# Kernel tuning notes

Measured on AMD Instinct MI355X. Metric: run time of the kernel, lower is better.

The kernel has to match this reference:

```python
import jax, jax.numpy as jnp
import numpy as np

N, E, IN, H0, H1 = 50000, 1600000, 64, 64, 128


def _gcn(h, W, b, row, col):
    # PyG GCNConv, add_self_loops=False, unit edge weights:
    # out[col] += d^{-1/2}[row] * d^{-1/2}[col] * (h @ W)[row]; bias added after aggregation
    n = h.shape[0]
    deg = jnp.zeros((n,), h.dtype).at[col].add(jnp.ones((row.shape[0],), h.dtype))
    dinv = jnp.where(deg > 0, jax.lax.rsqrt(jnp.maximum(deg, 1e-12)), 0.0)
    norm = (dinv[row] * dinv[col])[:, None]  # [E,1]
    m = h @ W  # transform before propagate (small GEMM)
    out = jnp.zeros((n, W.shape[1]), h.dtype).at[col].add(norm * m[row])
    return out + b


def _bn(h, g, b):
    # BatchNorm1d training-mode math (biased variance), eps=1e-5
    mu = h.mean(0)
    var = ((h - mu) ** 2).mean(0)
    return g * (h - mu) * jax.lax.rsqrt(var + 1e-5) + b


def _san(h):
    return jnp.nan_to_num(h, nan=0.0, posinf=100.0, neginf=-100.0)


def _slice(x, ei, W0, b0, W1, b1, res1, g0, be0, g1, be1):
    row, col = ei[0], ei[1]
    # layer 0: conv -> bn -> relu -> (dropout=eval identity) -> residual (Identity, 64==64) -> nan_to_num
    h1 = _san(jax.nn.relu(_bn(_gcn(x, W0, b0, row, col), g0, be0)) + x)
    # layer 1 (last): conv -> bn -> residual (Linear proj 64->128, no bias) -> nan_to_num
    h2 = _san(_bn(_gcn(h1, W1, b1, row, col), g1, be1) + h1 @ res1)
    return h2


def setup_inputs() -> dict:
    k = jax.random.split(jax.random.key(0), 16)
    f = lambda kk, sh, s: jax.random.normal(kk, sh, jnp.float32) * s
    return {
        "x": f(k[0], (N, IN), 1.0),
        "edge_index0": jax.random.randint(k[1], (2, E), 0, N),
        "edge_index1": jax.random.randint(k[2], (2, E), 0, N),
        "w0_s0": f(k[3], (IN, H0), 0.1), "b0_s0": jnp.zeros((H0,), jnp.float32),
        "w1_s0": f(k[4], (H0, H1), 0.1), "b1_s0": jnp.zeros((H1,), jnp.float32),
        "res1_s0": f(k[5], (H0, H1), 0.1),
        "w0_s1": f(k[6], (IN, H0), 0.1), "b0_s1": jnp.zeros((H0,), jnp.float32),
        "w1_s1": f(k[7], (H0, H1), 0.1), "b1_s1": jnp.zeros((H1,), jnp.float32),
        "res1_s1": f(k[8], (H0, H1), 0.1),
        "bn_g0": jnp.ones((H0,), jnp.float32), "bn_b0": jnp.zeros((H0,), jnp.float32),
        "bn_g1": jnp.ones((H1,), jnp.float32), "bn_b1": jnp.zeros((H1,), jnp.float32),
        "fc1_w": f(k[9], (2 * H1, H1), 0.1), "fc1_b": jnp.zeros((H1,), jnp.float32),
        "fc2_w": f(k[10], (H1, 2), 0.1), "fc2_b": jnp.zeros((2,), jnp.float32),
    }


def reference(x, edge_index0, edge_index1,
              w0_s0, b0_s0, w1_s0, b1_s0, res1_s0,
              w0_s1, b0_s1, w1_s1, b1_s1, res1_s1,
              bn_g0, bn_b0, bn_g1, bn_b1,
              fc1_w, fc1_b, fc2_w, fc2_b):
    out0 = _slice(x, edge_index0, w0_s0, b0_s0, w1_s0, b1_s0, res1_s0, bn_g0, bn_b0, bn_g1, bn_b1)
    out1 = _slice(x, edge_index1, w0_s1, b0_s1, w1_s1, b1_s1, res1_s1, bn_g0, bn_b0, bn_g1, bn_b1)
    combined = jnp.concatenate([out0, out1], axis=1)  # [N, 2*H1]
    h = jax.nn.relu(combined @ fc1_w + fc1_b)  # dropout is eval-mode identity
    logits = h @ fc2_w + fc2_b
    return logits, jax.nn.softmax(logits, axis=1)
```

## Files before the change

### kernel.cpp

```cpp
#include <hip/hip_runtime.h>
#include <hip/hip_bf16.h>
#include <math.h>


typedef short v8s __attribute__((ext_vector_type(8)));
typedef float f32x4 __attribute__((ext_vector_type(4)));

#define BSTRIDE 10240

__device__ __forceinline__ float sanf(float v) {
    if (v != v) return 0.f;
    if (isinf(v)) return v > 0.f ? 100.f : -100.f;
    return v;
}

__device__ __forceinline__ unsigned short bf16of(float v) {
    __hip_bfloat16 h = __float2bfloat16(v);
    return *(unsigned short*)&h;
}
__device__ __forceinline__ unsigned pack2(float lo, float hi) {
    return (unsigned)bf16of(lo) | ((unsigned)bf16of(hi) << 16);
}
__device__ __forceinline__ float uflo(unsigned u) { return __uint_as_float(u << 16); }
__device__ __forceinline__ float ufhi(unsigned u) { return __uint_as_float(u & 0xFFFF0000u); }
__device__ __forceinline__ float fofbf16(unsigned short u) {
    return __uint_as_float(((unsigned)u) << 16);
}

__device__ __forceinline__ void packone(const float* __restrict__ src, unsigned* __restrict__ dst,
                                        int L, int Khalf, int F) {
    int c = L / Khalf, kp = L - c * Khalf;
    dst[L] = pack2(src[(2 * kp) * F + c], src[(2 * kp + 1) * F + c]);
}

__global__ __launch_bounds__(256) void prep_kernel(const float* __restrict__ w0_0,
                                                   const float* __restrict__ w0_1,
                                                   const float* __restrict__ w1_0,
                                                   const float* __restrict__ w1_1,
                                                   const float* __restrict__ r_0,
                                                   const float* __restrict__ r_1,
                                                   const float* __restrict__ fc1,
                                                   unsigned* __restrict__ wpk,
                                                   int* __restrict__ bcnt,
                                                   float* __restrict__ sums) {
    int gid = blockIdx.x * 256 + threadIdx.x;
    if (gid < 512) bcnt[gid] = 0;
    if (gid < 8192) sums[gid] = 0.f;
    if (gid < 2048)       packone(w0_0, wpk + 0,     gid - 0,     32, 64);
    else if (gid < 4096)  packone(w0_1, wpk + 2048,  gid - 2048,  32, 64);
    else if (gid < 8192)  packone(w1_0, wpk + 4096,  gid - 4096,  32, 128);
    else if (gid < 12288) packone(w1_1, wpk + 8192,  gid - 8192,  32, 128);
    else if (gid < 16384) packone(r_0,  wpk + 12288, gid - 12288, 32, 128);
    else if (gid < 20480) packone(r_1,  wpk + 16384, gid - 16384, 32, 128);
    else if (gid < 36864) packone(fc1,  wpk + 20480, gid - 20480, 128, 128);
}


__global__ __launch_bounds__(512) void kC_bin(const int* __restrict__ ei0,
                                              const int* __restrict__ ei1,
                                              int* __restrict__ bcnt,
                                              unsigned* __restrict__ binned,
                                              int E, int n) {
    __shared__ int cnt[512];
    __shared__ int base[512];
    int t = threadIdx.x;
    cnt[t] = 0;
    int E2 = 2 * E;
    int e0 = blockIdx.x * 8192;
    unsigned pk[16];
    int bk[16];
    __syncthreads();
#pragma unroll
    for (int j = 0; j < 16; ++j) {
        int ge = e0 + t + j * 512;
        bk[j] = -1;
        if (ge < E2) {
            int slice = ge >= E;
            const int* ei = slice ? ei1 : ei0;
            int e = ge - slice * E;
            int col = ei[E + e], row = ei[e];
            int gcol = slice * n + col;
            bk[j] = gcol >> 8;
            pk[j] = (unsigned)row | (((unsigned)gcol & 255u) << 16);
            atomicAdd(&cnt[bk[j]], 1);
        }
    }
    __syncthreads();
    {
        int c = cnt[t];
        base[t] = c ? atomicAdd(&bcnt[t], c) : 0;
    }
    __syncthreads();
    cnt[t] = 0;
    __syncthreads();
#pragma unroll
    for (int j = 0; j < 16; ++j) {
        if (bk[j] >= 0) {
            int loc = atomicAdd(&cnt[bk[j]], 1);
            int off = base[bk[j]] + loc;
            if (off < BSTRIDE) binned[(size_t)bk[j] * BSTRIDE + off] = pk[j];
        }
    }
}

__global__ __launch_bounds__(256) void kB_scan(const int* __restrict__ bcnt,
                                               int* __restrict__ bstart, int NB) {
    __shared__ int tmp[256];
    int t = threadIdx.x, carry = 0;
    for (int bse = 0; bse < NB; bse += 256) {
        int i = bse + t;
        int v = (i < NB) ? bcnt[i] : 0;
        tmp[t] = v;
        __syncthreads();
        for (int off = 1; off < 256; off <<= 1) {
            int u = (t >= off) ? tmp[t - off] : 0;
            __syncthreads();
            tmp[t] += u;
            __syncthreads();
        }
        if (i < NB) bstart[i] = tmp[t] - v + carry;
        carry += tmp[255];
        __syncthreads();
    }
    if (t == 0) bstart[NB] = carry;
}

__global__ __launch_bounds__(512) void kD_build(const unsigned* __restrict__ binned,
                                                const int* __restrict__ bstart,
                                                int* __restrict__ rowptr,
                                                float* __restrict__ dinv,
                                                unsigned short* __restrict__ csr,
                                                int n2, int NB) {
    __shared__ int cnt[256];
    __shared__ int scn[256];
    __shared__ int cur[256];
    int b = blockIdx.x, t = threadIdx.x;
    int s = bstart[b], e = bstart[b + 1];
    int m = e - s;
    const unsigned* seg = binned + (size_t)b * BSTRIDE;
    if (t < 256) cnt[t] = 0;
    __syncthreads();
    for (int i = t; i < m; i += 512) atomicAdd(&cnt[(seg[i] >> 16) & 255], 1);
    __syncthreads();
    int v = (t < 256) ? cnt[t] : 0;
    if (t < 256) scn[t] = v;
    __syncthreads();
    for (int off = 1; off < 256; off <<= 1) {
        int u = (t < 256 && t >= off) ? scn[t - off] : 0;
        __syncthreads();
        if (t < 256) scn[t] += u;
        __syncthreads();
    }
    if (t < 256) {
        int excl = scn[t] - v;
        int gcol = b * 256 + t;
        if (gcol < n2) {
            rowptr[gcol] = s + excl;
            dinv[gcol] = v > 0 ? rsqrtf((float)v) : 0.f;
        }
        cur[t] = excl;
    }
    __syncthreads();
    for (int i = t; i < m; i += 512) {
        unsigned p = seg[i];
        int cl = (p >> 16) & 255;
        int pos = s + atomicAdd(&cur[cl], 1);
        csr[pos] = (unsigned short)(p & 0xFFFFu);
    }
    if (b == 0 && t == 0) rowptr[n2] = bstart[NB];
}


__global__ __launch_bounds__(256) void prescale_bf(const float* __restrict__ x,
                                                   const float* __restrict__ dinv,
                                                   unsigned short* __restrict__ xsb,
                                                   int n64, int n) {
    int i8 = (blockIdx.x * 256 + threadIdx.x) * 8;
    if (i8 >= n64) return;
    int row = i8 >> 6;
    float4 v0 = *(const float4*)&x[i8];
    float4 v1 = *(const float4*)&x[i8 + 4];
    float d0 = dinv[row], d1 = dinv[n + row];
    uint4 o0, o1;
    o0.x = pack2(v0.x * d0, v0.y * d0); o0.y = pack2(v0.z * d0, v0.w * d0);
    o0.z = pack2(v1.x * d0, v1.y * d0); o0.w = pack2(v1.z * d0, v1.w * d0);
    o1.x = pack2(v0.x * d1, v0.y * d1); o1.y = pack2(v0.z * d1, v0.w * d1);
    o1.z = pack2(v1.x * d1, v1.y * d1); o1.w = pack2(v1.z * d1, v1.w * d1);
    *(uint4*)&xsb[i8] = o0;
    *(uint4*)&xsb[n64 + i8] = o1;
}

#define LOAD8(U, IDX)                                                       \
    do {                                                                    \
        _Pragma("unroll") for (int j = 0; j < 8; ++j) {                     \
            int r = __shfl((IDX), j, 8);                                    \
            (U)[j] = *(const uint4*)&mb[(size_t)r * 64 + l * 8];            \
        }                                                                   \
    } while (0)
#define ZPAD8(U, BB)                                                        \
    do {                                                                    \
        _Pragma("unroll") for (int j = 0; j < 8; ++j)                       \
            if ((BB) + j >= e) { (U)[j].x = 0; (U)[j].y = 0;                \
                                 (U)[j].z = 0; (U)[j].w = 0; }              \
    } while (0)
#define ACC8(U)                                                             \
    do {                                                                    \
        _Pragma("unroll") for (int j = 0; j < 8; ++j) {                     \
            a0 += uflo((U)[j].x); a1 += ufhi((U)[j].x);                     \
            a2 += uflo((U)[j].y); a3 += ufhi((U)[j].y);                     \
            a4 += uflo((U)[j].z); a5 += ufhi((U)[j].z);                     \
            a6 += uflo((U)[j].w); a7 += ufhi((U)[j].w);                     \
        }                                                                   \
    } while (0)

__global__ __launch_bounds__(256) void gatherbf_kernel(const int* __restrict__ rowptr,
                                                       const unsigned short* __restrict__ csr,
                                                       const unsigned short* __restrict__ xsb,
                                                       const float* __restrict__ dinv,
                                                       unsigned short* __restrict__ outb,
                                                       int n) {
    int blk = blockIdx.x;
    int xcd = blk & 7;
    int slice = (xcd >= 4) ? 1 : 0;
    int rank = (blk >> 3) * 4 + (xcd & 3);
    int nodeLocal = rank * 32 + (threadIdx.x >> 3);
    if (nodeLocal >= n) return;
    int node = slice * n + nodeLocal;
    int l = threadIdx.x & 7;
    const unsigned short* mb = xsb + (size_t)slice * n * 64;
    int s = rowptr[node], e = rowptr[node + 1];
    float a0 = 0.f, a1 = 0.f, a2 = 0.f, a3 = 0.f, a4 = 0.f, a5 = 0.f, a6 = 0.f, a7 = 0.f;
    uint4 uA[8], uB[8];
    int b = s;
    if (b + 8 <= e) {
        int ia = csr[b + l];
        LOAD8(uA, ia);
        int bB = b + 8;
        int ib = (bB + l < e) ? (int)csr[bB + l] : 0;
        while (true) {
            bool hasB = (bB < e);
            if (hasB) {
                LOAD8(uB, ib);
                if (bB + 8 > e) ZPAD8(uB, bB);
            }
            int bA2 = bB + 8;
            if (bA2 < e) ia = (bA2 + l < e) ? (int)csr[bA2 + l] : 0;
            ACC8(uA);
            if (!hasB) break;
            bool hasA2 = (bA2 < e);
            if (hasA2) {
                LOAD8(uA, ia);
                if (bA2 + 8 > e) ZPAD8(uA, bA2);
            }
            int bB2 = bA2 + 8;
            if (bB2 < e) ib = (bB2 + l < e) ? (int)csr[bB2 + l] : 0;
            ACC8(uB);
            if (!hasA2) break;
            bB = bB2;
        }
    } else if (b < e) {
        int ia = (b + l < e) ? (int)csr[b + l] : 0;
        LOAD8(uA, ia);
        ZPAD8(uA, b);
        ACC8(uA);
    }
    float d = dinv[node];
    uint4 o;
    o.x = pack2(a0 * d, a1 * d);
    o.y = pack2(a2 * d, a3 * d);
    o.z = pack2(a4 * d, a5 * d);
    o.w = pack2(a6 * d, a7 * d);
    *(uint4*)&outb[(size_t)node * 64 + l * 8] = o;
}


template <int F>
__global__ __launch_bounds__(256) void mfma_gemmb(const unsigned short* __restrict__ Ab,
                                                  const unsigned* __restrict__ WT0,
                                                  const unsigned* __restrict__ WT1,
                                                  unsigned short* __restrict__ Cb,
                                                  float* __restrict__ sums_base,
                                                  int roff, int n) {
    constexpr int NC = F / 16;
    __shared__ float ls[2 * F];
    __shared__ unsigned short stb[64 * F];
    int BPS = (n + 63) >> 6;
    int slice = blockIdx.x >= BPS;
    int sb = blockIdx.x - slice * BPS;
    const unsigned* WT = slice ? WT1 : WT0;
    int row0 = slice * n + sb * 64;
    int rows = min(64, n - sb * 64);
    for (int i = threadIdx.x; i < 2 * F; i += 256) ls[i] = 0.f;
    int w = threadIdx.x >> 6, lane = threadIdx.x & 63, q = lane >> 4, ln = lane & 15;
    const unsigned* A32 = (const unsigned*)Ab;
    size_t arow = (size_t)(row0 + 16 * w + ln) * 32;
    v8s af0 = *(const v8s*)&A32[arow + q * 4];
    v8s af1 = *(const v8s*)&A32[arow + 16 + q * 4];
    f32x4 acc[NC];
#pragma unroll
    for (int ct = 0; ct < NC; ++ct) acc[ct] = {0.f, 0.f, 0.f, 0.f};
#pragma unroll
    for (int ct = 0; ct < NC; ++ct) {
        v8s b0 = *(const v8s*)&WT[(ct * 16 + ln) * 32 + q * 4];
        v8s b1 = *(const v8s*)&WT[(ct * 16 + ln) * 32 + 16 + q * 4];
        acc[ct] = __builtin_amdgcn_mfma_f32_16x16x32_bf16(af0, b0, acc[ct], 0, 0, 0);
        acc[ct] = __builtin_amdgcn_mfma_f32_16x16x32_bf16(af1, b1, acc[ct], 0, 0, 0);
    }
    __syncthreads();
#pragma unroll
    for (int ct = 0; ct < NC; ++ct) {
        float s1 = 0.f, s2 = 0.f;
        int cc = ct * 16 + ln;
#pragma unroll
        for (int i = 0; i < 4; ++i) {
            int r = 16 * w + q * 4 + i;
            stb[r * F + (cc ^ ((r & 7) << 3))] = bf16of(acc[ct][i]);
            if (r < rows) {
                float v = acc[ct][i];
                s1 += v;
                s2 += v * v;
            }
        }
        s1 += __shfl_xor(s1, 16); s1 += __shfl_xor(s1, 32);
        s2 += __shfl_xor(s2, 16); s2 += __shfl_xor(s2, 32);
        if (q == 0) {
            atomicAdd(&ls[cc], s1);
            atomicAdd(&ls[F + cc], s2);
        }
    }
    __syncthreads();
    {
        constexpr int CPT = F / 4;
        int rr = threadIdx.x >> 2, sg = threadIdx.x & 3;
        if (rr < rows) {
            int swz = (rr & 7) << 3;
            int cb = sg * CPT;
            uint4* dst = (uint4*)(Cb + (size_t)(row0 + rr) * F + cb);
#pragma unroll
            for (int jj = 0; jj < CPT / 8; ++jj)
                dst[jj] = *(const uint4*)&stb[rr * F + ((cb + jj * 8) ^ swz)];
        }
    }
    if (threadIdx.x < F) {
        float* dst = sums_base + (blockIdx.x & 7) * 1024 + roff + slice * 2 * F;
        unsafeAtomicAdd(&dst[threadIdx.x], ls[threadIdx.x]);
        unsafeAtomicAdd(&dst[F + threadIdx.x], ls[F + threadIdx.x]);
    }
}

__global__ __launch_bounds__(256) void mfma_apply1(const unsigned short* __restrict__ h1b,
                                                   const unsigned short* __restrict__ Tb,
                                                   const unsigned* __restrict__ RT0,
                                                   const unsigned* __restrict__ RT1,
                                                   const float* __restrict__ scsh,
                                                   unsigned short* __restrict__ comb, int n) {
    __shared__ float st[64 * 128];
    int BPS = (n + 63) >> 6;
    int slice = blockIdx.x >= BPS;
    int sb = blockIdx.x - slice * BPS;
    const unsigned* WT = slice ? RT1 : RT0;
    int row0 = slice * n + sb * 64;
    int rows = min(64, n - sb * 64);
    int w = threadIdx.x >> 6, lane = threadIdx.x & 63, q = lane >> 4, ln = lane & 15;
    const unsigned* A32 = (const unsigned*)h1b;
    size_t arow = (size_t)(row0 + 16 * w + ln) * 32;
    v8s af0 = *(const v8s*)&A32[arow + q * 4];
    v8s af1 = *(const v8s*)&A32[arow + 16 + q * 4];
    f32x4 acc[8];
#pragma unroll
    for (int ct = 0; ct < 8; ++ct) acc[ct] = {0.f, 0.f, 0.f, 0.f};
#pragma unroll
    for (int ct = 0; ct < 8; ++ct) {
        v8s b0 = *(const v8s*)&WT[(ct * 16 + ln) * 32 + q * 4];
        v8s b1 = *(const v8s*)&WT[(ct * 16 + ln) * 32 + 16 + q * 4];
        acc[ct] = __builtin_amdgcn_mfma_f32_16x16x32_bf16(af0, b0, acc[ct], 0, 0, 0);
        acc[ct] = __builtin_amdgcn_mfma_f32_16x16x32_bf16(af1, b1, acc[ct], 0, 0, 0);
    }
#pragma unroll
    for (int ct = 0; ct < 8; ++ct) {
        int cc = ct * 16 + ln;
#pragma unroll
        for (int i = 0; i < 4; ++i) {
            int r = 16 * w + q * 4 + i;
            st[r * 128 + (cc ^ ((r & 7) << 2))] = acc[ct][i];
        }
    }
    __syncthreads();
    int rr = threadIdx.x >> 2, sg = threadIdx.x & 3;
    if (rr >= rows) return;
    int swz = (rr & 7) << 2;
    int rg = row0 + rr;
    const uint4* tbp = (const uint4*)(Tb + (size_t)rg * 128 + sg * 32);
    const float* scb = scsh + slice * 256 + sg * 32;
    uint4* outp = (uint4*)(comb + (size_t)(rg - slice * n) * 256 + slice * 128 + sg * 32);
#pragma unroll
    for (int jj = 0; jj < 4; ++jj) {
        uint4 t = tbp[jj];
        int base = sg * 32 + jj * 8;
        float4 a0 = *(const float4*)&st[rr * 128 + (base ^ swz)];
        float4 a1 = *(const float4*)&st[rr * 128 + ((base + 4) ^ swz)];
        float4 s0 = *(const float4*)&scb[jj * 8];
        float4 s1 = *(const float4*)&scb[jj * 8 + 4];
        float4 h0 = *(const float4*)&scb[128 + jj * 8];
        float4 h1v = *(const float4*)&scb[128 + jj * 8 + 4];
        float o0 = sanf(fmaf(uflo(t.x), s0.x, h0.x) + a0.x);
        float o1 = sanf(fmaf(ufhi(t.x), s0.y, h0.y) + a0.y);
        float o2 = sanf(fmaf(uflo(t.y), s0.z, h0.z) + a0.z);
        float o3 = sanf(fmaf(ufhi(t.y), s0.w, h0.w) + a0.w);
        float o4 = sanf(fmaf(uflo(t.z), s1.x, h1v.x) + a1.x);
        float o5 = sanf(fmaf(ufhi(t.z), s1.y, h1v.y) + a1.y);
        float o6 = sanf(fmaf(uflo(t.w), s1.z, h1v.z) + a1.z);
        float o7 = sanf(fmaf(ufhi(t.w), s1.w, h1v.w) + a1.w);
        uint4 ov;
        ov.x = pack2(o0, o1);
        ov.y = pack2(o2, o3);
        ov.z = pack2(o4, o5);
        ov.w = pack2(o6, o7);
        outp[jj] = ov;
    }
}

__global__ __launch_bounds__(256) void mfma_head_fc2(const unsigned short* __restrict__ comb,
                                                     const unsigned* __restrict__ FT,
                                                     const float* __restrict__ bias,
                                                     const float* __restrict__ w2,
                                                     const float* __restrict__ b2,
                                                     float* __restrict__ out, int n) {
    int row0 = blockIdx.x * 64;
    int rows = min(64, n - row0);
    int w = threadIdx.x >> 6, lane = threadIdx.x & 63, q = lane >> 4, ln = lane & 15;
    const unsigned* A32 = (const unsigned*)comb;
    size_t arow = (size_t)(row0 + 16 * w + ln) * 128;
    f32x4 acc[8];
#pragma unroll
    for (int ct = 0; ct < 8; ++ct) acc[ct] = {0.f, 0.f, 0.f, 0.f};
#pragma unroll
    for (int kt = 0; kt < 4; ++kt) {
        v8s af0 = *(const v8s*)&A32[arow + kt * 32 + q * 4];
        v8s af1 = *(const v8s*)&A32[arow + kt * 32 + 16 + q * 4];
#pragma unroll
        for (int ct = 0; ct < 8; ++ct) {
            v8s b0 = *(const v8s*)&FT[(ct * 16 + ln) * 128 + kt * 32 + q * 4];
            v8s b1 = *(const v8s*)&FT[(ct * 16 + ln) * 128 + kt * 32 + 16 + q * 4];
            acc[ct] = __builtin_amdgcn_mfma_f32_16x16x32_bf16(af0, b0, acc[ct], 0, 0, 0);
            acc[ct] = __builtin_amdgcn_mfma_f32_16x16x32_bf16(af1, b1, acc[ct], 0, 0, 0);
        }
    }
    float p0[4] = {0.f, 0.f, 0.f, 0.f}, p1[4] = {0.f, 0.f, 0.f, 0.f};
#pragma unroll
    for (int ct = 0; ct < 8; ++ct) {
        int c = ct * 16 + ln;
        float bi = bias[c];
        float w20 = w2[c * 2], w21 = w2[c * 2 + 1];
#pragma unroll
        for (int i = 0; i < 4; ++i) {
            float h = fmaxf(acc[ct][i] + bi, 0.f);
            p0[i] = fmaf(h, w20, p0[i]);
            p1[i] = fmaf(h, w21, p1[i]);
        }
    }
#pragma unroll
    for (int i = 0; i < 4; ++i) {
#pragma unroll
        for (int msk = 1; msk < 16; msk <<= 1) {
            p0[i] += __shfl_xor(p0[i], msk);
            p1[i] += __shfl_xor(p1[i], msk);
        }
    }
    if (ln == 0) {
        float bb0 = b2[0], bb1 = b2[1];
#pragma unroll
        for (int i = 0; i < 4; ++i) {
            int r = 16 * w + q * 4 + i;
            if (r >= rows) continue;
            int R = row0 + r;
            float l0 = p0[i] + bb0, l1 = p1[i] + bb1;
            float mx = fmaxf(l0, l1);
            float e0 = expf(l0 - mx), e1 = expf(l1 - mx);
            float inv = 1.0f / (e0 + e1);
            out[(size_t)R * 2] = l0;
            out[(size_t)R * 2 + 1] = l1;
            out[(size_t)2 * n + R * 2] = e0 * inv;
            out[(size_t)2 * n + R * 2 + 1] = e1 * inv;
        }
    }
}


template <int F>
__global__ void bnfinal_kernel(const float* __restrict__ sums_base, int roff,
                               const float* __restrict__ g,
                               const float* __restrict__ be, float* __restrict__ scsh, int n) {
    int f = threadIdx.x;
    if (f >= F) return;
    int slice = blockIdx.x;
    float s1 = 0.f, s2 = 0.f;
#pragma unroll
    for (int r = 0; r < 8; ++r) {
        const float* src = sums_base + r * 1024 + roff + slice * 2 * F;
        s1 += src[f];
        s2 += src[F + f];
    }
    float inv_n = 1.0f / (float)n;
    float mu = s1 * inv_n;
    float var = fmaxf(s2 * inv_n - mu * mu, 0.f);
    float scale = g[f] * rsqrtf(var + 1e-5f);
    scsh[slice * 2 * F + f] = scale;
    scsh[slice * 2 * F + F + f] = be[f] - mu * scale;
}

__global__ __launch_bounds__(256) void apply0_kernel(const unsigned short* __restrict__ t0b,
                                                     const float* __restrict__ x,
                                                     const float* __restrict__ scsh,
                                                     const float* __restrict__ dinv,
                                                     unsigned short* __restrict__ h1b,
                                                     unsigned short* __restrict__ h1sb,
                                                     int n64, int total) {
    int i8 = (blockIdx.x * 256 + threadIdx.x) * 8;
    if (i8 >= total) return;
    int slice = i8 >= n64;
    int f0 = i8 & 63;
    const float* sc = scsh + slice * 128;
    uint4 t = *(const uint4*)&t0b[i8];
    const float* xp = x + (i8 - slice * n64);
    float4 x0 = *(const float4*)xp;
    float4 x1 = *(const float4*)(xp + 4);
    float4 s0 = *(const float4*)&sc[f0];
    float4 s1 = *(const float4*)&sc[f0 + 4];
    float4 g0 = *(const float4*)&sc[64 + f0];
    float4 g1 = *(const float4*)&sc[64 + f0 + 4];
    float d = dinv[i8 >> 6];
    float tv[8] = {uflo(t.x), ufhi(t.x), uflo(t.y), ufhi(t.y),
                   uflo(t.z), ufhi(t.z), uflo(t.w), ufhi(t.w)};
    float sa[8] = {s0.x, s0.y, s0.z, s0.w, s1.x, s1.y, s1.z, s1.w};
    float sh[8] = {g0.x, g0.y, g0.z, g0.w, g1.x, g1.y, g1.z, g1.w};
    float xv[8] = {x0.x, x0.y, x0.z, x0.w, x1.x, x1.y, x1.z, x1.w};
    unsigned po[4], ps[4];
#pragma unroll
    for (int j = 0; j < 4; ++j) {
        float a = sanf(fmaxf(fmaf(tv[2 * j], sa[2 * j], sh[2 * j]), 0.f) + xv[2 * j]);
        float b = sanf(fmaxf(fmaf(tv[2 * j + 1], sa[2 * j + 1], sh[2 * j + 1]), 0.f) + xv[2 * j + 1]);
        po[j] = pack2(a, b);
        ps[j] = pack2(a * d, b * d);
    }
    *(uint4*)&h1b[i8] = *(uint4*)po;
    *(uint4*)&h1sb[i8] = *(uint4*)ps;
}

static inline int cdiv(int a, int b) { return (a + b - 1) / b; }

extern "C" void kernel_launch(void* const* d_in, const int* in_sizes, int n_in,
                              void* d_out, int out_size, void* d_ws, size_t ws_size,
                              hipStream_t stream) {
    const float* x       = (const float*)d_in[0];
    const int*   ei0     = (const int*)d_in[1];
    const int*   ei1     = (const int*)d_in[2];
    const float* w0_s0   = (const float*)d_in[3];
    const float* w1_s0   = (const float*)d_in[5];
    const float* res1_s0 = (const float*)d_in[7];
    const float* w0_s1   = (const float*)d_in[8];
    const float* w1_s1   = (const float*)d_in[10];
    const float* res1_s1 = (const float*)d_in[12];
    const float* bn_g0   = (const float*)d_in[13];
    const float* bn_b0   = (const float*)d_in[14];
    const float* bn_g1   = (const float*)d_in[15];
    const float* bn_b1   = (const float*)d_in[16];
    const float* fc1_w   = (const float*)d_in[17];
    const float* fc1_b   = (const float*)d_in[18];
    const float* fc2_w   = (const float*)d_in[19];
    const float* fc2_b   = (const float*)d_in[20];
    float* out = (float*)d_out;

    int n = in_sizes[0] / 64;
    int E = in_sizes[1] / 2;
    int n2 = 2 * n, E2 = 2 * E;
    int n64 = n * 64;
    int NB = cdiv(n2, 256);
    int BPS = cdiv(n, 64);
    int GB = 8 * cdiv(cdiv(n, 32), 4);

    float* X1 = (float*)d_ws;
    float* S  = X1 + (size_t)n2 * 64;
    unsigned short* Gb   = (unsigned short*)(S + (size_t)n2 * 64);
    unsigned short* h1b  = Gb + (size_t)n2 * 64;
    unsigned short* comb = h1b + (size_t)n2 * 64;
    unsigned short* xsb  = comb + (size_t)n * 256;
    float* dinv = (float*)(xsb + (size_t)n * 128);
    float* sums = dinv + n2;
    float* scsh = sums + 8192;
    unsigned* wpk = (unsigned*)(scsh + 512);
    unsigned short* csr = (unsigned short*)(wpk + 36864);
    int* rowptr = (int*)(csr + (size_t)E2);
    int* bcnt   = rowptr + (n2 + 1);
    int* bstart = bcnt + 512;
    unsigned short* t0b = (unsigned short*)X1;
    unsigned short* Tb  = (unsigned short*)X1;
    unsigned* binned = (unsigned*)comb;
    unsigned short* h1sb = (unsigned short*)S;
    unsigned* w0T0 = wpk + 0,    *w0T1 = wpk + 2048;
    unsigned* w1T0 = wpk + 4096, *w1T1 = wpk + 8192;
    unsigned* rT0  = wpk + 12288,*rT1  = wpk + 16384;
    unsigned* fT   = wpk + 20480;

    prep_kernel<<<144, 256, 0, stream>>>(w0_s0, w0_s1, w1_s0, w1_s1,
                                         res1_s0, res1_s1, fc1_w, wpk, bcnt, sums);
    kC_bin<<<cdiv(E2, 8192), 512, 0, stream>>>(ei0, ei1, bcnt, binned, E, n);
    kB_scan<<<1, 256, 0, stream>>>(bcnt, bstart, NB);
    kD_build<<<NB, 512, 0, stream>>>(binned, bstart, rowptr, dinv, csr, n2, NB);

    prescale_bf<<<cdiv(n64, 2048), 256, 0, stream>>>(x, dinv, xsb, n64, n);
    gatherbf_kernel<<<GB, 256, 0, stream>>>(rowptr, csr, xsb, dinv, Gb, n);
    mfma_gemmb<64><<<2 * BPS, 256, 0, stream>>>(Gb, w0T0, w0T1, t0b, sums, 512, n);
    bnfinal_kernel<64><<<2, 64, 0, stream>>>(sums, 512, bn_g0, bn_b0, scsh, n);
    apply0_kernel<<<cdiv(2 * n64, 2048), 256, 0, stream>>>(t0b, x, scsh, dinv, h1b, h1sb, n64, 2 * n64);

    gatherbf_kernel<<<GB, 256, 0, stream>>>(rowptr, csr, h1sb, dinv, Gb, n);
    mfma_gemmb<128><<<2 * BPS, 256, 0, stream>>>(Gb, w1T0, w1T1, Tb, sums, 0, n);
    bnfinal_kernel<128><<<2, 128, 0, stream>>>(sums, 0, bn_g1, bn_b1, scsh, n);
    mfma_apply1<<<2 * BPS, 256, 0, stream>>>(h1b, Tb, rT0, rT1, scsh, comb, n);

    mfma_head_fc2<<<BPS, 256, 0, stream>>>(comb, fT, fc1_b, fc2_w, fc2_b, out, n);
}
```

Before: 363.8 us.

## Fuse gather into GEMM, fold scan into CSR build and BN finalize into consumers

The edge gather now writes its aggregated tile into LDS and feeds the MFMA GEMM directly, so the bf16 intermediate no longer round-trips through global memory. The single-block bucket scan kernel is removed: every kD_build block recomputes a 512-entry prefix over the bucket counts. The BatchNorm finalize kernels are also removed; apply0 and apply1 compute scale and shift from the partial sums themselves. Together these cut five launches and one global buffer pass, at the cost of redundant per-block prefix and stat work and more LDS per GEMM block, which may lower occupancy.

```diff
diff --git a/kernel.cpp b/kernel.cpp
--- a/kernel.cpp
+++ b/kernel.cpp
@@ -103,39 +103,27 @@
     }
 }
 
-__global__ __launch_bounds__(256) void kB_scan(const int* __restrict__ bcnt,
-                                               int* __restrict__ bstart, int NB) {
-    __shared__ int tmp[256];
-    int t = threadIdx.x, carry = 0;
-    for (int bse = 0; bse < NB; bse += 256) {
-        int i = bse + t;
-        int v = (i < NB) ? bcnt[i] : 0;
-        tmp[t] = v;
-        __syncthreads();
-        for (int off = 1; off < 256; off <<= 1) {
-            int u = (t >= off) ? tmp[t - off] : 0;
-            __syncthreads();
-            tmp[t] += u;
-            __syncthreads();
-        }
-        if (i < NB) bstart[i] = tmp[t] - v + carry;
-        carry += tmp[255];
-        __syncthreads();
-    }
-    if (t == 0) bstart[NB] = carry;
-}
-
 __global__ __launch_bounds__(512) void kD_build(const unsigned* __restrict__ binned,
-                                                const int* __restrict__ bstart,
+                                                const int* __restrict__ bcnt,
                                                 int* __restrict__ rowptr,
                                                 float* __restrict__ dinv,
                                                 unsigned short* __restrict__ csr,
                                                 int n2, int NB) {
+    __shared__ int pref[512];
     __shared__ int cnt[256];
     __shared__ int scn[256];
     __shared__ int cur[256];
     int b = blockIdx.x, t = threadIdx.x;
-    int s = bstart[b], e = bstart[b + 1];
+    pref[t] = (t < NB) ? bcnt[t] : 0;
+    __syncthreads();
+    for (int off = 1; off < 512; off <<= 1) {
+        int u = (t >= off) ? pref[t - off] : 0;
+        __syncthreads();
+        pref[t] += u;
+        __syncthreads();
+    }
+    int s = (b > 0) ? pref[b - 1] : 0;
+    int e = pref[b];
     int m = e - s;
     const unsigned* seg = binned + (size_t)b * BSTRIDE;
     if (t < 256) cnt[t] = 0;
@@ -167,7 +155,7 @@
         int pos = s + atomicAdd(&cur[cl], 1);
         csr[pos] = (unsigned short)(p & 0xFFFFu);
     }
-    if (b == 0 && t == 0) rowptr[n2] = bstart[NB];
+    if (b == 0 && t == 0) rowptr[n2] = pref[NB - 1];
 }
 
 
@@ -213,21 +201,12 @@
         }                                                                   \
     } while (0)
 
-__global__ __launch_bounds__(256) void gatherbf_kernel(const int* __restrict__ rowptr,
-                                                       const unsigned short* __restrict__ csr,
-                                                       const unsigned short* __restrict__ xsb,
-                                                       const float* __restrict__ dinv,
-                                                       unsigned short* __restrict__ outb,
-                                                       int n) {
-    int blk = blockIdx.x;
-    int xcd = blk & 7;
-    int slice = (xcd >= 4) ? 1 : 0;
-    int rank = (blk >> 3) * 4 + (xcd & 3);
-    int nodeLocal = rank * 32 + (threadIdx.x >> 3);
-    if (nodeLocal >= n) return;
-    int node = slice * n + nodeLocal;
-    int l = threadIdx.x & 7;
-    const unsigned short* mb = xsb + (size_t)slice * n * 64;
+__device__ __forceinline__ void gather_node(const int* __restrict__ rowptr,
+                                            const unsigned short* __restrict__ csr,
+                                            const unsigned short* __restrict__ mb,
+                                            const float* __restrict__ dinv,
+                                            int node, int l,
+                                            unsigned short* __restrict__ dstrow) {
     int s = rowptr[node], e = rowptr[node + 1];
     float a0 = 0.f, a1 = 0.f, a2 = 0.f, a3 = 0.f, a4 = 0.f, a5 = 0.f, a6 = 0.f, a7 = 0.f;
     uint4 uA[8], uB[8];
@@ -270,32 +249,49 @@
     o.y = pack2(a2 * d, a3 * d);
     o.z = pack2(a4 * d, a5 * d);
     o.w = pack2(a6 * d, a7 * d);
-    *(uint4*)&outb[(size_t)node * 64 + l * 8] = o;
-}
-
+    *(uint4*)&dstrow[l * 8] = o;
+}
 
 template <int F>
-__global__ __launch_bounds__(256) void mfma_gemmb(const unsigned short* __restrict__ Ab,
-                                                  const unsigned* __restrict__ WT0,
-                                                  const unsigned* __restrict__ WT1,
-                                                  unsigned short* __restrict__ Cb,
-                                                  float* __restrict__ sums_base,
-                                                  int roff, int n) {
+__global__ __launch_bounds__(256) void gather_gemmb(const int* __restrict__ rowptr,
+                                                    const unsigned short* __restrict__ csr,
+                                                    const unsigned short* __restrict__ xsb,
+                                                    const float* __restrict__ dinv,
+                                                    const unsigned* __restrict__ WT0,
+                                                    const unsigned* __restrict__ WT1,
+                                                    unsigned short* __restrict__ Cb,
+                                                    float* __restrict__ sums_base,
+                                                    int roff, int n, int BPS) {
     constexpr int NC = F / 16;
+    __shared__ unsigned short at[64 * 72];
+    __shared__ unsigned short stb[64 * F];
     __shared__ float ls[2 * F];
-    __shared__ unsigned short stb[64 * F];
-    int BPS = (n + 63) >> 6;
-    int slice = blockIdx.x >= BPS;
-    int sb = blockIdx.x - slice * BPS;
+    int blk = blockIdx.x;
+    int xcd = blk & 7;
+    int slice = (xcd >= 4) ? 1 : 0;
+    int sb = (blk >> 3) * 4 + (xcd & 3);
+    if (sb >= BPS) return;
     const unsigned* WT = slice ? WT1 : WT0;
     int row0 = slice * n + sb * 64;
     int rows = min(64, n - sb * 64);
+    int grp = threadIdx.x >> 3, l = threadIdx.x & 7;
+    const unsigned short* mb = xsb + (size_t)slice * n * 64;
+#pragma unroll
+    for (int half = 0; half < 2; ++half) {
+        int lr = grp + half * 32;
+        if (lr < rows) {
+            gather_node(rowptr, csr, mb, dinv, row0 + lr, l, &at[lr * 72]);
+        } else {
+            uint4 z; z.x = 0; z.y = 0; z.z = 0; z.w = 0;
+            *(uint4*)&at[lr * 72 + l * 8] = z;
+        }
+    }
     for (int i = threadIdx.x; i < 2 * F; i += 256) ls[i] = 0.f;
+    __syncthreads();
     int w = threadIdx.x >> 6, lane = threadIdx.x & 63, q = lane >> 4, ln = lane & 15;
-    const unsigned* A32 = (const unsigned*)Ab;
-    size_t arow = (size_t)(row0 + 16 * w + ln) * 32;
-    v8s af0 = *(const v8s*)&A32[arow + q * 4];
-    v8s af1 = *(const v8s*)&A32[arow + 16 + q * 4];
+    int arow = (16 * w + ln) * 72;
+    v8s af0 = *(const v8s*)&at[arow + q * 8];
+    v8s af1 = *(const v8s*)&at[arow + 32 + q * 8];
     f32x4 acc[NC];
 #pragma unroll
     for (int ct = 0; ct < NC; ++ct) acc[ct] = {0.f, 0.f, 0.f, 0.f};
@@ -306,7 +302,6 @@
         acc[ct] = __builtin_amdgcn_mfma_f32_16x16x32_bf16(af0, b0, acc[ct], 0, 0, 0);
         acc[ct] = __builtin_amdgcn_mfma_f32_16x16x32_bf16(af1, b1, acc[ct], 0, 0, 0);
     }
-    __syncthreads();
 #pragma unroll
     for (int ct = 0; ct < NC; ++ct) {
         float s1 = 0.f, s2 = 0.f;
@@ -352,16 +347,35 @@
                                                    const unsigned short* __restrict__ Tb,
                                                    const unsigned* __restrict__ RT0,
                                                    const unsigned* __restrict__ RT1,
-                                                   const float* __restrict__ scsh,
+                                                   const float* __restrict__ sums_base,
+                                                   const float* __restrict__ g,
+                                                   const float* __restrict__ be,
                                                    unsigned short* __restrict__ comb, int n) {
     __shared__ float st[64 * 128];
+    __shared__ float scl[256];
     int BPS = (n + 63) >> 6;
     int slice = blockIdx.x >= BPS;
     int sb = blockIdx.x - slice * BPS;
     const unsigned* WT = slice ? RT1 : RT0;
     int row0 = slice * n + sb * 64;
     int rows = min(64, n - sb * 64);
-    int w = threadIdx.x >> 6, lane = threadIdx.x & 63, q = lane >> 4, ln = lane & 15;
+    int t = threadIdx.x;
+    if (t < 128) {
+        float s1 = 0.f, s2 = 0.f;
+#pragma unroll
+        for (int r = 0; r < 8; ++r) {
+            const float* src = sums_base + r * 1024 + slice * 256;
+            s1 += src[t];
+            s2 += src[128 + t];
+        }
+        float inv_n = 1.0f / (float)n;
+        float mu = s1 * inv_n;
+        float var = fmaxf(s2 * inv_n - mu * mu, 0.f);
+        float scale = g[t] * rsqrtf(var + 1e-5f);
+        scl[t] = scale;
+        scl[128 + t] = be[t] - mu * scale;
+    }
+    int w = t >> 6, lane = t & 63, q = lane >> 4, ln = lane & 15;
     const unsigned* A32 = (const unsigned*)h1b;
     size_t arow = (size_t)(row0 + 16 * w + ln) * 32;
     v8s af0 = *(const v8s*)&A32[arow + q * 4];
@@ -386,16 +400,16 @@
         }
     }
     __syncthreads();
-    int rr = threadIdx.x >> 2, sg = threadIdx.x & 3;
+    int rr = t >> 2, sg = t & 3;
     if (rr >= rows) return;
     int swz = (rr & 7) << 2;
     int rg = row0 + rr;
     const uint4* tbp = (const uint4*)(Tb + (size_t)rg * 128 + sg * 32);
-    const float* scb = scsh + slice * 256 + sg * 32;
+    const float* scb = scl + sg * 32;
     uint4* outp = (uint4*)(comb + (size_t)(rg - slice * n) * 256 + slice * 128 + sg * 32);
 #pragma unroll
     for (int jj = 0; jj < 4; ++jj) {
-        uint4 t = tbp[jj];
+        uint4 tv = tbp[jj];
         int base = sg * 32 + jj * 8;
         float4 a0 = *(const float4*)&st[rr * 128 + (base ^ swz)];
         float4 a1 = *(const float4*)&st[rr * 128 + ((base + 4) ^ swz)];
@@ -403,14 +417,14 @@
         float4 s1 = *(const float4*)&scb[jj * 8 + 4];
         float4 h0 = *(const float4*)&scb[128 + jj * 8];
         float4 h1v = *(const float4*)&scb[128 + jj * 8 + 4];
-        float o0 = sanf(fmaf(uflo(t.x), s0.x, h0.x) + a0.x);
-        float o1 = sanf(fmaf(ufhi(t.x), s0.y, h0.y) + a0.y);
-        float o2 = sanf(fmaf(uflo(t.y), s0.z, h0.z) + a0.z);
-        float o3 = sanf(fmaf(ufhi(t.y), s0.w, h0.w) + a0.w);
-        float o4 = sanf(fmaf(uflo(t.z), s1.x, h1v.x) + a1.x);
-        float o5 = sanf(fmaf(ufhi(t.z), s1.y, h1v.y) + a1.y);
-        float o6 = sanf(fmaf(uflo(t.w), s1.z, h1v.z) + a1.z);
-        float o7 = sanf(fmaf(ufhi(t.w), s1.w, h1v.w) + a1.w);
+        float o0 = sanf(fmaf(uflo(tv.x), s0.x, h0.x) + a0.x);
+        float o1 = sanf(fmaf(ufhi(tv.x), s0.y, h0.y) + a0.y);
+        float o2 = sanf(fmaf(uflo(tv.y), s0.z, h0.z) + a0.z);
+        float o3 = sanf(fmaf(ufhi(tv.y), s0.w, h0.w) + a0.w);
+        float o4 = sanf(fmaf(uflo(tv.z), s1.x, h1v.x) + a1.x);
+        float o5 = sanf(fmaf(ufhi(tv.z), s1.y, h1v.y) + a1.y);
+        float o6 = sanf(fmaf(uflo(tv.w), s1.z, h1v.z) + a1.z);
+        float o7 = sanf(fmaf(ufhi(tv.w), s1.w, h1v.w) + a1.w);
         uint4 ov;
         ov.x = pack2(o0, o1);
         ov.y = pack2(o2, o3);
@@ -486,60 +500,58 @@
     }
 }
 
-
-template <int F>
-__global__ void bnfinal_kernel(const float* __restrict__ sums_base, int roff,
-                               const float* __restrict__ g,
-                               const float* __restrict__ be, float* __restrict__ scsh, int n) {
-    int f = threadIdx.x;
-    if (f >= F) return;
-    int slice = blockIdx.x;
-    float s1 = 0.f, s2 = 0.f;
-#pragma unroll
-    for (int r = 0; r < 8; ++r) {
-        const float* src = sums_base + r * 1024 + roff + slice * 2 * F;
-        s1 += src[f];
-        s2 += src[F + f];
-    }
-    float inv_n = 1.0f / (float)n;
-    float mu = s1 * inv_n;
-    float var = fmaxf(s2 * inv_n - mu * mu, 0.f);
-    float scale = g[f] * rsqrtf(var + 1e-5f);
-    scsh[slice * 2 * F + f] = scale;
-    scsh[slice * 2 * F + F + f] = be[f] - mu * scale;
-}
-
 __global__ __launch_bounds__(256) void apply0_kernel(const unsigned short* __restrict__ t0b,
                                                      const float* __restrict__ x,
-                                                     const float* __restrict__ scsh,
+                                                     const float* __restrict__ sums_base,
+                                                     const float* __restrict__ g,
+                                                     const float* __restrict__ be,
                                                      const float* __restrict__ dinv,
                                                      unsigned short* __restrict__ h1b,
                                                      unsigned short* __restrict__ h1sb,
-                                                     int n64, int total) {
-    int i8 = (blockIdx.x * 256 + threadIdx.x) * 8;
+                                                     int n64, int total, int n) {
+    __shared__ float sc[256];
+    int t = threadIdx.x;
+    if (t < 128) {
+        int slice = t >> 6, f = t & 63;
+        float s1 = 0.f, s2 = 0.f;
+#pragma unroll
+        for (int r = 0; r < 8; ++r) {
+            const float* src = sums_base + r * 1024 + 512 + slice * 128;
+            s1 += src[f];
+            s2 += src[64 + f];
+        }
+        float inv_n = 1.0f / (float)n;
+        float mu = s1 * inv_n;
+        float var = fmaxf(s2 * inv_n - mu * mu, 0.f);
+        float scale = g[f] * rsqrtf(var + 1e-5f);
+        sc[slice * 128 + f] = scale;
+        sc[slice * 128 + 64 + f] = be[f] - mu * scale;
+    }
+    __syncthreads();
+    int i8 = (blockIdx.x * 256 + t) * 8;
     if (i8 >= total) return;
     int slice = i8 >= n64;
     int f0 = i8 & 63;
-    const float* sc = scsh + slice * 128;
-    uint4 t = *(const uint4*)&t0b[i8];
+    const float* scp = sc + slice * 128;
+    uint4 tv = *(const uint4*)&t0b[i8];
     const float* xp = x + (i8 - slice * n64);
     float4 x0 = *(const float4*)xp;
     float4 x1 = *(const float4*)(xp + 4);
-    float4 s0 = *(const float4*)&sc[f0];
-    float4 s1 = *(const float4*)&sc[f0 + 4];
-    float4 g0 = *(const float4*)&sc[64 + f0];
-    float4 g1 = *(const float4*)&sc[64 + f0 + 4];
+    float4 s0 = *(const float4*)&scp[f0];
+    float4 s1 = *(const float4*)&scp[f0 + 4];
+    float4 g0 = *(const float4*)&scp[64 + f0];
+    float4 g1 = *(const float4*)&scp[64 + f0 + 4];
     float d = dinv[i8 >> 6];
-    float tv[8] = {uflo(t.x), ufhi(t.x), uflo(t.y), ufhi(t.y),
-                   uflo(t.z), ufhi(t.z), uflo(t.w), ufhi(t.w)};
+    float tvv[8] = {uflo(tv.x), ufhi(tv.x), uflo(tv.y), ufhi(tv.y),
+                    uflo(tv.z), ufhi(tv.z), uflo(tv.w), ufhi(tv.w)};
     float sa[8] = {s0.x, s0.y, s0.z, s0.w, s1.x, s1.y, s1.z, s1.w};
     float sh[8] = {g0.x, g0.y, g0.z, g0.w, g1.x, g1.y, g1.z, g1.w};
     float xv[8] = {x0.x, x0.y, x0.z, x0.w, x1.x, x1.y, x1.z, x1.w};
     unsigned po[4], ps[4];
 #pragma unroll
     for (int j = 0; j < 4; ++j) {
-        float a = sanf(fmaxf(fmaf(tv[2 * j], sa[2 * j], sh[2 * j]), 0.f) + xv[2 * j]);
-        float b = sanf(fmaxf(fmaf(tv[2 * j + 1], sa[2 * j + 1], sh[2 * j + 1]), 0.f) + xv[2 * j + 1]);
+        float a = sanf(fmaxf(fmaf(tvv[2 * j], sa[2 * j], sh[2 * j]), 0.f) + xv[2 * j]);
+        float b = sanf(fmaxf(fmaf(tvv[2 * j + 1], sa[2 * j + 1], sh[2 * j + 1]), 0.f) + xv[2 * j + 1]);
         po[j] = pack2(a, b);
         ps[j] = pack2(a * d, b * d);
     }
@@ -577,7 +589,7 @@
     int n64 = n * 64;
     int NB = cdiv(n2, 256);
     int BPS = cdiv(n, 64);
-    int GB = 8 * cdiv(cdiv(n, 32), 4);
+    int GG = 8 * cdiv(BPS, 4);
 
     float* X1 = (float*)d_ws;
     float* S  = X1 + (size_t)n2 * 64;
@@ -592,7 +604,6 @@
     unsigned short* csr = (unsigned short*)(wpk + 36864);
     int* rowptr = (int*)(csr + (size_t)E2);
     int* bcnt   = rowptr + (n2 + 1);
-    int* bstart = bcnt + 512;
     unsigned short* t0b = (unsigned short*)X1;
     unsigned short* Tb  = (unsigned short*)X1;
     unsigned* binned = (unsigned*)comb;
@@ -605,19 +616,17 @@
     prep_kernel<<<144, 256, 0, stream>>>(w0_s0, w0_s1, w1_s0, w1_s1,
                                          res1_s0, res1_s1, fc1_w, wpk, bcnt, sums);
     kC_bin<<<cdiv(E2, 8192), 512, 0, stream>>>(ei0, ei1, bcnt, binned, E, n);
-    kB_scan<<<1, 256, 0, stream>>>(bcnt, bstart, NB);
-    kD_build<<<NB, 512, 0, stream>>>(binned, bstart, rowptr, dinv, csr, n2, NB);
+    kD_build<<<NB, 512, 0, stream>>>(binned, bcnt, rowptr, dinv, csr, n2, NB);
 
     prescale_bf<<<cdiv(n64, 2048), 256, 0, stream>>>(x, dinv, xsb, n64, n);
-    gatherbf_kernel<<<GB, 256, 0, stream>>>(rowptr, csr, xsb, dinv, Gb, n);
-    mfma_gemmb<64><<<2 * BPS, 256, 0, stream>>>(Gb, w0T0, w0T1, t0b, sums, 512, n);
-    bnfinal_kernel<64><<<2, 64, 0, stream>>>(sums, 512, bn_g0, bn_b0, scsh, n);
-    apply0_kernel<<<cdiv(2 * n64, 2048), 256, 0, stream>>>(t0b, x, scsh, dinv, h1b, h1sb, n64, 2 * n64);
-
-    gatherbf_kernel<<<GB, 256, 0, stream>>>(rowptr, csr, h1sb, dinv, Gb, n);
-    mfma_gemmb<128><<<2 * BPS, 256, 0, stream>>>(Gb, w1T0, w1T1, Tb, sums, 0, n);
-    bnfinal_kernel<128><<<2, 128, 0, stream>>>(sums, 0, bn_g1, bn_b1, scsh, n);
-    mfma_apply1<<<2 * BPS, 256, 0, stream>>>(h1b, Tb, rT0, rT1, scsh, comb, n);
+    gather_gemmb<64><<<GG, 256, 0, stream>>>(rowptr, csr, xsb, dinv, w0T0, w0T1,
+                                             t0b, sums, 512, n, BPS);
+    apply0_kernel<<<cdiv(2 * n64, 2048), 256, 0, stream>>>(t0b, x, sums, bn_g0, bn_b0,
+                                                           dinv, h1b, h1sb, n64, 2 * n64, n);
+
+    gather_gemmb<128><<<GG, 256, 0, stream>>>(rowptr, csr, h1sb, dinv, w1T0, w1T1,
+                                              Tb, sums, 0, n, BPS);
+    mfma_apply1<<<2 * BPS, 256, 0, stream>>>(h1b, Tb, rT0, rT1, sums, bn_g1, bn_b1, comb, n);
 
     mfma_head_fc2<<<BPS, 256, 0, stream>>>(comb, fT, fc1_b, fc2_w, fc2_b, out, n);
 }
```

Measured after the change: 371.1 us. 1.02x slower.
